# Kernel tuning notes

Measured on AMD Instinct MI355X. Metric: run time of the kernel, lower is better.

## Reference

```python
import jax, jax.numpy as jnp
import numpy as np

# ---- static tree structure (matches the 4-ary adjacency passed at init) ----
N = 145  # total nodes incl. root 0; output has N-1 = 144 channels
PARENT = np.array([(i - 1) // 4 for i in range(1, N)], dtype=np.int64)  # parent node id of node i (i=1..N-1)
DEPTH = np.zeros(N, dtype=np.int64)
for i in range(1, N):
    DEPTH[i] = DEPTH[(i - 1) // 4] + 1
MAX_DEPTH = int(DEPTH.max())
PARENT_J = jnp.asarray(PARENT)          # [N-1] segment id (= parent node) per non-root node
DEPTH_J = jnp.asarray(DEPTH[1:])        # [N-1] depth of each non-root node (>=1)


def tree_softmax(x):
    """x: [B, N-1, H, W] logits. Sibling-group softmax along channel axis,
    then multiply each node's prob by the product of its ancestors' probs."""
    xt = jnp.moveaxis(x, 1, 0)  # [N-1, B, H, W]: node axis leading for segment ops
    seg = PARENT_J
    # segmented (per-sibling-group) numerically stable softmax
    m = jax.ops.segment_max(xt, seg, num_segments=N)[seg]
    e = jnp.exp(xt - m)
    s = jax.ops.segment_sum(e, seg, num_segments=N)[seg]
    p = e / s  # [N-1, B, H, W]
    # level-by-level multiplicative propagation: res[i] = p[i] * res[parent(i)]
    res = p  # depth-1 nodes (root children) are already final
    for d in range(2, MAX_DEPTH + 1):
        # pad with ones at node 0 (root) so we can gather by node id
        resp = jnp.concatenate([jnp.ones_like(res[:1]), res], axis=0)  # [N, B, H, W]
        gathered = resp[PARENT_J]  # each node's parent's (already-final) result
        mask = (DEPTH_J == d).reshape(-1, 1, 1, 1)
        res = jnp.where(mask, res * gathered, res)
    return jnp.moveaxis(res, 0, 1)  # [B, N-1, H, W]


def setup_inputs() -> dict:
    key = jax.random.key(0)
    x = jax.random.normal(key, (4, 144, 256, 256), dtype=jnp.float32)
    return {"x": x}


def reference(x):
    return tree_softmax(x)
```

## Files before the change

kernel.cpp:

```cpp
#include <hip/hip_runtime.h>


__device__ __forceinline__ void grp4s(float a, float b, float c, float d,
                                      float pr, float out[4]) {
    float m = fmaxf(fmaxf(a, b), fmaxf(c, d));
    float e0 = __expf(a - m);
    float e1 = __expf(b - m);
    float e2 = __expf(c - m);
    float e3 = __expf(d - m);
    float f = pr / (e0 + e1 + e2 + e3);
    out[0] = e0 * f;
    out[1] = e1 * f;
    out[2] = e2 * f;
    out[3] = e3 * f;
}

__global__ __launch_bounds__(256, 1) void tree_softmax_kernel(
        const float* __restrict__ x, float* __restrict__ y) {
    const int HW = 256 * 256;
    const int C  = 144;

    int tid = blockIdx.x * 256 + threadIdx.x;
    int b   = tid >> 16;
    int rem = tid & 65535;
    size_t base = (size_t)b * C * HW + (size_t)rem;

    const float* __restrict__ xp = x + base;
    float*       __restrict__ yp = y + base;

    float v[144];
#pragma unroll
    for (int c = 0; c < 144; ++c) v[c] = xp[c * HW];

    float o[4];

    float r1[4];
    grp4s(v[0], v[1], v[2], v[3], 1.0f, r1);
#pragma unroll
    for (int c = 0; c < 4; ++c) __builtin_nontemporal_store(r1[c], &yp[c * HW]);

    float r2[16];
#pragma unroll
    for (int p = 0; p < 4; ++p) {
        grp4s(v[4 + 4 * p], v[5 + 4 * p], v[6 + 4 * p], v[7 + 4 * p], r1[p], o);
#pragma unroll
        for (int c = 0; c < 4; ++c) {
            __builtin_nontemporal_store(o[c], &yp[(4 + 4 * p + c) * HW]);
            r2[4 * p + c] = o[c];
        }
    }

    float keep[15];
#pragma unroll
    for (int p = 0; p < 16; ++p) {
        int c0 = 20 + 4 * p;
        grp4s(v[c0], v[c0 + 1], v[c0 + 2], v[c0 + 3], r2[p], o);
#pragma unroll
        for (int c = 0; c < 4; ++c) {
            int idx = 4 * p + c;
            __builtin_nontemporal_store(o[c], &yp[(c0 + c) * HW]);
            if (idx < 15) keep[idx] = o[c];
        }
    }

#pragma unroll
    for (int p = 0; p < 15; ++p) {
        int c0 = 84 + 4 * p;
        grp4s(v[c0], v[c0 + 1], v[c0 + 2], v[c0 + 3], keep[p], o);
#pragma unroll
        for (int c = 0; c < 4; ++c)
            __builtin_nontemporal_store(o[c], &yp[(c0 + c) * HW]);
    }
}

extern "C" void kernel_launch(void* const* d_in, const int* in_sizes, int n_in,
                              void* d_out, int out_size, void* d_ws, size_t ws_size,
                              hipStream_t stream) {
    const float* x = (const float*)d_in[0];
    float* y = (float*)d_out;
    const int threads = 256;
    const int blocks  = (4 * 256 * 256) / threads;
    tree_softmax_kernel<<<blocks, threads, 0, stream>>>(x, y);
}
```

Before: 259.4 us.

## Stage inputs through LDS via direct global-to-LDS loads with 64-thread blocks

Each thread no longer holds all 144 channel values in registers. The loads now go straight from global memory into LDS through global_load_lds, and the per-group softmax reads its operands back from LDS. Blocks shrink to a single 64-thread wavefront that uses about 36 KB of LDS, which cuts register pressure and should let more waves stay resident to hide memory latency. The cost is LDS occupancy limits, extra LDS reads, and a full vmcnt(0) wait before any compute can begin.

```diff
diff --git a/kernel.cpp b/kernel.cpp
--- a/kernel.cpp
+++ b/kernel.cpp
@@ -1,5 +1,8 @@
 #include <hip/hip_runtime.h>
 
+
+typedef const __attribute__((address_space(1))) float gfloat;
+typedef __attribute__((address_space(3))) float lfloat;
 
 __device__ __forceinline__ void grp4s(float a, float b, float c, float d,
                                       float pr, float out[4]) {
@@ -15,37 +18,47 @@
     out[3] = e3 * f;
 }
 
-__global__ __launch_bounds__(256, 1) void tree_softmax_kernel(
+__global__ __launch_bounds__(64) void tree_softmax_kernel(
         const float* __restrict__ x, float* __restrict__ y) {
-    const int HW = 256 * 256;
+    __shared__ float lds[144 * 64];
+    const int HW = 65536;
     const int C  = 144;
 
-    int tid = blockIdx.x * 256 + threadIdx.x;
-    int b   = tid >> 16;
-    int rem = tid & 65535;
-    size_t base = (size_t)b * C * HW + (size_t)rem;
+    const int t    = threadIdx.x;
+    const int blk  = blockIdx.x;
+    const int b    = blk >> 10;
+    const int pix0 = (blk & 1023) << 6;
+    const size_t base = (size_t)b * C * HW + (size_t)pix0;
 
-    const float* __restrict__ xp = x + base;
-    float*       __restrict__ yp = y + base;
+    const float* __restrict__ xg = x + base + t;
+    float*       __restrict__ yg = y + base + t;
 
-    float v[144];
 #pragma unroll
-    for (int c = 0; c < 144; ++c) v[c] = xp[c * HW];
+    for (int c = 0; c < 144; ++c) {
+        __builtin_amdgcn_global_load_lds(
+            (gfloat*)(xg + (size_t)c * HW),
+            (lfloat*)(&lds[c * 64]),
+            4, 0, 0);
+    }
+    asm volatile("s_waitcnt vmcnt(0)" ::: "memory");
+    __builtin_amdgcn_sched_barrier(0);
 
+#define L(c) lds[(c) * 64 + t]
     float o[4];
 
     float r1[4];
-    grp4s(v[0], v[1], v[2], v[3], 1.0f, r1);
+    grp4s(L(0), L(1), L(2), L(3), 1.0f, r1);
 #pragma unroll
-    for (int c = 0; c < 4; ++c) __builtin_nontemporal_store(r1[c], &yp[c * HW]);
+    for (int c = 0; c < 4; ++c) __builtin_nontemporal_store(r1[c], &yg[c * HW]);
 
     float r2[16];
 #pragma unroll
     for (int p = 0; p < 4; ++p) {
-        grp4s(v[4 + 4 * p], v[5 + 4 * p], v[6 + 4 * p], v[7 + 4 * p], r1[p], o);
+        int c0 = 4 + 4 * p;
+        grp4s(L(c0), L(c0 + 1), L(c0 + 2), L(c0 + 3), r1[p], o);
 #pragma unroll
         for (int c = 0; c < 4; ++c) {
-            __builtin_nontemporal_store(o[c], &yp[(4 + 4 * p + c) * HW]);
+            __builtin_nontemporal_store(o[c], &yg[(c0 + c) * HW]);
             r2[4 * p + c] = o[c];
         }
     }
@@ -54,11 +67,11 @@
 #pragma unroll
     for (int p = 0; p < 16; ++p) {
         int c0 = 20 + 4 * p;
-        grp4s(v[c0], v[c0 + 1], v[c0 + 2], v[c0 + 3], r2[p], o);
+        grp4s(L(c0), L(c0 + 1), L(c0 + 2), L(c0 + 3), r2[p], o);
 #pragma unroll
         for (int c = 0; c < 4; ++c) {
             int idx = 4 * p + c;
-            __builtin_nontemporal_store(o[c], &yp[(c0 + c) * HW]);
+            __builtin_nontemporal_store(o[c], &yg[(c0 + c) * HW]);
             if (idx < 15) keep[idx] = o[c];
         }
     }
@@ -66,11 +79,12 @@
 #pragma unroll
     for (int p = 0; p < 15; ++p) {
         int c0 = 84 + 4 * p;
-        grp4s(v[c0], v[c0 + 1], v[c0 + 2], v[c0 + 3], keep[p], o);
+        grp4s(L(c0), L(c0 + 1), L(c0 + 2), L(c0 + 3), keep[p], o);
 #pragma unroll
         for (int c = 0; c < 4; ++c)
-            __builtin_nontemporal_store(o[c], &yp[(c0 + c) * HW]);
+            __builtin_nontemporal_store(o[c], &yg[(c0 + c) * HW]);
     }
+#undef L
 }
 
 extern "C" void kernel_launch(void* const* d_in, const int* in_sizes, int n_in,
@@ -78,7 +92,7 @@
                               hipStream_t stream) {
     const float* x = (const float*)d_in[0];
     float* y = (float*)d_out;
-    const int threads = 256;
-    const int blocks  = (4 * 256 * 256) / threads;
+    const int threads = 64;
+    const int blocks  = (4 * 256 * 256) / 64;
     tree_softmax_kernel<<<blocks, threads, 0, stream>>>(x, y);
 }
```

Result: no change. 262.3 us (+1.1%).

## Stream channels through double-buffered LDS with async global_load_lds per wave

Applied to the files above, without the earlier changes.

Replaces the load-all-144-channels-into-registers approach with a per-wave pipeline that streams 16-channel chunks from global memory straight into a double-buffered LDS tile using global_load_lds. Manual vmcnt waits overlap the next chunks' loads with softmax compute on the current chunk. Only the parent probabilities still needed are kept in registers, which cuts register pressure and raises the launch-bounds occupancy target from 1 to 4 blocks. Stores switch from nontemporal to ordinary stores. The hand-written waitcnt counts depend on how many loads and stores are in flight, so correctness and timing rest on the compiler's instruction ordering.

```diff
diff --git a/kernel.cpp b/kernel.cpp
--- a/kernel.cpp
+++ b/kernel.cpp
@@ -1,75 +1,79 @@
 #include <hip/hip_runtime.h>
 
 
-__device__ __forceinline__ void grp4s(float a, float b, float c, float d,
-                                      float pr, float out[4]) {
-    float m = fmaxf(fmaxf(a, b), fmaxf(c, d));
-    float e0 = __expf(a - m);
-    float e1 = __expf(b - m);
-    float e2 = __expf(c - m);
-    float e3 = __expf(d - m);
-    float f = pr / (e0 + e1 + e2 + e3);
-    out[0] = e0 * f;
-    out[1] = e1 * f;
-    out[2] = e2 * f;
-    out[3] = e3 * f;
-}
+typedef const __attribute__((address_space(1))) float gfloat;
+typedef __attribute__((address_space(3))) float lfloat;
 
-__global__ __launch_bounds__(256, 1) void tree_softmax_kernel(
+__global__ __launch_bounds__(256, 4) void tree_softmax_kernel(
         const float* __restrict__ x, float* __restrict__ y) {
-    const int HW = 256 * 256;
-    const int C  = 144;
+    constexpr int HW  = 65536;
+    constexpr int C   = 144;
+    constexpr int CH  = 16;
+    constexpr int NCH = 9;
 
-    int tid = blockIdx.x * 256 + threadIdx.x;
-    int b   = tid >> 16;
-    int rem = tid & 65535;
-    size_t base = (size_t)b * C * HW + (size_t)rem;
+    __shared__ float lds[4][2][CH][64];
 
-    const float* __restrict__ xp = x + base;
-    float*       __restrict__ yp = y + base;
+    const int t     = threadIdx.x & 63;
+    const int w     = threadIdx.x >> 6;
+    const int gwave = blockIdx.x * 4 + w;
+    const int b     = gwave >> 10;
+    const int pix0  = (gwave & 1023) << 6;
+    const size_t base = (size_t)b * C * HW + (size_t)pix0;
 
-    float v[144];
-#pragma unroll
-    for (int c = 0; c < 144; ++c) v[c] = xp[c * HW];
-
-    float o[4];
-
-    float r1[4];
-    grp4s(v[0], v[1], v[2], v[3], 1.0f, r1);
-#pragma unroll
-    for (int c = 0; c < 4; ++c) __builtin_nontemporal_store(r1[c], &yp[c * HW]);
-
-    float r2[16];
-#pragma unroll
-    for (int p = 0; p < 4; ++p) {
-        grp4s(v[4 + 4 * p], v[5 + 4 * p], v[6 + 4 * p], v[7 + 4 * p], r1[p], o);
-#pragma unroll
-        for (int c = 0; c < 4; ++c) {
-            __builtin_nontemporal_store(o[c], &yp[(4 + 4 * p + c) * HW]);
-            r2[4 * p + c] = o[c];
-        }
-    }
-
-    float keep[15];
-#pragma unroll
-    for (int p = 0; p < 16; ++p) {
-        int c0 = 20 + 4 * p;
-        grp4s(v[c0], v[c0 + 1], v[c0 + 2], v[c0 + 3], r2[p], o);
-#pragma unroll
-        for (int c = 0; c < 4; ++c) {
-            int idx = 4 * p + c;
-            __builtin_nontemporal_store(o[c], &yp[(c0 + c) * HW]);
-            if (idx < 15) keep[idx] = o[c];
-        }
-    }
+    const float* __restrict__ xg = x + base + t;
+    float*       __restrict__ yg = y + base + t;
 
 #pragma unroll
-    for (int p = 0; p < 15; ++p) {
-        int c0 = 84 + 4 * p;
-        grp4s(v[c0], v[c0 + 1], v[c0 + 2], v[c0 + 3], keep[p], o);
+    for (int c = 0; c < CH; ++c)
+        __builtin_amdgcn_global_load_lds((gfloat*)(xg + (size_t)c * HW),
+                                         (lfloat*)&lds[w][0][c][0], 4, 0, 0);
 #pragma unroll
-        for (int c = 0; c < 4; ++c)
-            __builtin_nontemporal_store(o[c], &yp[(c0 + c) * HW]);
+    for (int c = 0; c < CH; ++c)
+        __builtin_amdgcn_global_load_lds((gfloat*)(xg + (size_t)(CH + c) * HW),
+                                         (lfloat*)&lds[w][1][c][0], 4, 0, 0);
+
+    float par[35];
+
+#pragma unroll
+    for (int k = 0; k < NCH; ++k) {
+        if (k == 0 || k == NCH - 1)
+            asm volatile("s_waitcnt vmcnt(16)" ::: "memory");
+        else
+            asm volatile("s_waitcnt vmcnt(32)" ::: "memory");
+
+#pragma unroll
+        for (int g = 0; g < 4; ++g) {
+            const int n  = k * 4 + g;
+            const int c0 = 4 * n;
+            float a0 = lds[w][k & 1][4 * g + 0][t];
+            float a1 = lds[w][k & 1][4 * g + 1][t];
+            float a2 = lds[w][k & 1][4 * g + 2][t];
+            float a3 = lds[w][k & 1][4 * g + 3][t];
+            float pr = (n == 0) ? 1.0f : par[n - 1];
+            float m  = fmaxf(fmaxf(a0, a1), fmaxf(a2, a3));
+            float e0 = __expf(a0 - m);
+            float e1 = __expf(a1 - m);
+            float e2 = __expf(a2 - m);
+            float e3 = __expf(a3 - m);
+            float f  = pr / (e0 + e1 + e2 + e3);
+            float o0 = e0 * f, o1 = e1 * f, o2 = e2 * f, o3 = e3 * f;
+            yg[(size_t)(c0 + 0) * HW] = o0;
+            yg[(size_t)(c0 + 1) * HW] = o1;
+            yg[(size_t)(c0 + 2) * HW] = o2;
+            yg[(size_t)(c0 + 3) * HW] = o3;
+            if (c0 + 0 < 35) par[c0 + 0] = o0;
+            if (c0 + 1 < 35) par[c0 + 1] = o1;
+            if (c0 + 2 < 35) par[c0 + 2] = o2;
+            if (c0 + 3 < 35) par[c0 + 3] = o3;
+        }
+
+        if (k + 2 < NCH) {
+#pragma unroll
+            for (int c = 0; c < CH; ++c)
+                __builtin_amdgcn_global_load_lds(
+                    (gfloat*)(xg + (size_t)((k + 2) * CH + c) * HW),
+                    (lfloat*)&lds[w][k & 1][c][0], 4, 0, 0);
+        }
     }
 }
 
@@ -79,6 +83,6 @@
     const float* x = (const float*)d_in[0];
     float* y = (float*)d_out;
     const int threads = 256;
-    const int blocks  = (4 * 256 * 256) / threads;
+    const int blocks  = (4 * 256 * 256) / (64 * 4);
     tree_softmax_kernel<<<blocks, threads, 0, stream>>>(x, y);
 }
```

New measurement: 255.4 us. About the same (-1.6%).
